# Kernel optimization log

Measured on AMD Instinct MI355X. Metric: run time of the kernel, lower is better.

Reference implementation:

```python
import jax, jax.numpy as jnp
import numpy as np
from jax import lax

R = 3
D = (2 * R + 1) ** 2  # 49 local offsets


def _unfold(x, r):
    # torch F.unfold(kernel=2r+1, padding=r): (B,C,H,W) -> (B, C*K*K, H, W),
    # channel-major (c, ky, kx) ordering, matching conv_general_dilated_patches.
    k = 2 * r + 1
    return lax.conv_general_dilated_patches(
        x, (k, k), (1, 1), [(r, r), (r, r)],
        dimension_numbers=("NCHW", "OIHW", "NCHW"))


def _l2norm(x, eps=1e-12):
    n = jnp.sqrt(jnp.sum(x * x, axis=1, keepdims=True))
    return x / jnp.maximum(n, eps)


def setup_inputs() -> dict:
    key = jax.random.key(0)
    ks = jax.random.split(key, 8)
    B, Cin, Cmid, H, W = 2, 256, 128, 112, 112
    phi_cur = jax.random.normal(ks[0], (B, Cin, H, W), jnp.float32)
    phi_rnd = jax.random.normal(ks[1], (B, Cin, H, W), jnp.float32)
    P_cur = jax.random.normal(ks[2], (B, 3, H, W), jnp.float32)
    P_rnd = jax.random.normal(ks[3], (B, 3, H, W), jnp.float32)
    Wq = jax.random.normal(ks[4], (Cmid, Cin), jnp.float32) * 0.05
    Wk = jax.random.normal(ks[5], (Cmid, Cin), jnp.float32) * 0.05
    Wv = jax.random.normal(ks[6], (D, D), jnp.float32) * 0.1
    bv = jnp.zeros((D,), jnp.float32)
    gamma = jnp.array(1.0, jnp.float32)
    return dict(phi_cur=phi_cur, phi_rnd=phi_rnd, P_cur=P_cur, P_rnd=P_rnd,
                Wq=Wq, Wk=Wk, Wv=Wv, bv=bv, gamma=gamma)


def reference(phi_cur, phi_rnd, P_cur, P_rnd, Wq, Wk, Wv, bv, gamma):
    B, _, H, W = phi_cur.shape
    # 1x1 convs + channel L2 normalize
    q = _l2norm(jnp.einsum('oc,bchw->bohw', Wq, phi_cur))
    k = _l2norm(jnp.einsum('oc,bchw->bohw', Wk, phi_rnd))
    # local cost volume: patches (B, Cmid, D, H, W)
    patches = _unfold(k, R).reshape(B, -1, D, H, W)
    corr = jnp.einsum('bchw,bcdhw->bdhw', q, patches)  # (B,D,H,W)
    vol_corr = jnp.einsum('ed,bdhw->behw', Wv, corr) + bv[None, :, None, None]
    # geometric bias
    Pr = _unfold(P_rnd, R).reshape(B, 3, D, H, W)
    dP = P_cur[:, :, None, :, :] - Pr  # (B,3,D,H,W)
    dz = dP[:, 2]
    dist = jnp.sqrt(jnp.clip(jnp.sum(dP * dP, axis=1), 1e-12, None))
    logits = vol_corr + gamma * (-dist - 0.5 * jnp.abs(dz))
    w = jax.nn.softmax(logits, axis=1)
    off = jnp.arange(-R, R + 1, dtype=w.dtype)
    dY, dX = jnp.meshgrid(off, off, indexing='ij')
    offx = dX.reshape(1, D, 1, 1)
    offy = dY.reshape(1, D, 1, 1)
    du = jnp.sum(w * offx, axis=1, keepdims=True)
    dv = jnp.sum(w * offy, axis=1, keepdims=True)
    conf = jnp.max(w, axis=1, keepdims=True)
    return du, dv, conf
```

## Files before the change

### kernel.cpp

```cpp
#include <hip/hip_runtime.h>
#include <hip/hip_bf16.h>
#include <math.h>

constexpr int B    = 2;
constexpr int CIN  = 256;
constexpr int CMID = 128;
constexpr int H    = 112;
constexpr int W    = 112;
constexpr int HW   = H * W;
constexpr int NPIX = B * HW;
constexpr int RAD  = 3;
constexpr int KS   = 7;
constexpr int DD   = 49;

typedef __attribute__((ext_vector_type(8))) short  short8;
typedef __attribute__((ext_vector_type(4))) float  float4v;

__device__ __forceinline__ unsigned pkbf(float a, float b) {
    __hip_bfloat162 h = __float22bfloat162_rn(make_float2(a, b));
    union { __hip_bfloat162 h2; unsigned u; } c;
    c.h2 = h;
    return c.u;
}

__global__ __launch_bounds__(256) void prep(
    const float* __restrict__ Wq, const float* __restrict__ Wk,
    const float* __restrict__ Wv,
    unsigned short* __restrict__ wqb, unsigned short* __restrict__ wkb,
    float* __restrict__ wvp)
{
    if (blockIdx.x < 64) {
        const int i  = blockIdx.x * 256 + threadIdx.x;
        const int n4 = (CMID * CIN) / 4;
        const float4 v = (i < n4) ? ((const float4*)Wq)[i] : ((const float4*)Wk)[i - n4];
        uint2 r;
        r.x = pkbf(v.x, v.y);
        r.y = pkbf(v.z, v.w);
        if (i < n4) ((uint2*)wqb)[i] = r;
        else        ((uint2*)wkb)[i - n4] = r;
    } else {
        for (int idx = threadIdx.x; idx < DD * 52; idx += 256) {
            const int r = idx / 52, c = idx % 52;
            wvp[idx] = (c < DD) ? Wv[r * DD + c] : 0.f;
        }
    }
}

constexpr int PSTR = 264;

__global__ __launch_bounds__(256, 4) void proj_mfma(
    const float* __restrict__ phi_cur, const float* __restrict__ phi_rnd,
    const unsigned short* __restrict__ wq_bf, const unsigned short* __restrict__ wk_bf,
    unsigned short* __restrict__ q_ws, unsigned short* __restrict__ k_ws)
{
    __shared__ unsigned short pt[64 * PSTR];
    __shared__ float red[4][64];

    const int tid  = threadIdx.x;
    const int lane = tid & 63;
    const int wv   = __builtin_amdgcn_readfirstlane(tid >> 6);
    const int t    = blockIdx.y;

    const float* __restrict__ phi          = t ? phi_rnd : phi_cur;
    const unsigned short* __restrict__ Wbf = t ? wk_bf : wq_bf;
    unsigned short* __restrict__ outp      = t ? k_ws : q_ws;

    const int pgb = blockIdx.x * 64;
    const int b   = pgb / HW;
    const int pim = pgb % HW;
    const float* pbase = phi + (size_t)b * CIN * HW + pim;

    const int m = lane & 15, quad = lane >> 4;

    short8 af[2][8];
#pragma unroll
    for (int ot = 0; ot < 2; ++ot)
#pragma unroll
        for (int kc = 0; kc < 8; ++kc)
            af[ot][kc] = *(const short8*)(Wbf +
                (size_t)(wv * 32 + ot * 16 + m) * CIN + kc * 32 + quad * 8);

#pragma unroll
    for (int half = 0; half < 2; ++half) {
        float4 va[4], vb[4];
#pragma unroll
        for (int p = 0; p < 4; ++p) {
            const int idx = (half * 4 + p) * 256 + tid;
            const int cp  = idx >> 4;
            const int pq  = idx & 15;
            const int c0  = cp * 2;
            va[p] = *(const float4*)(pbase + (size_t)c0 * HW + pq * 4);
            vb[p] = *(const float4*)(pbase + (size_t)(c0 + 1) * HW + pq * 4);
        }
#pragma unroll
        for (int p = 0; p < 4; ++p) {
            const int idx = (half * 4 + p) * 256 + tid;
            const int cp  = idx >> 4;
            const int pq  = idx & 15;
            const int c0  = cp * 2;
            const int swz = ((pq >> 1) & 3) << 3;
            const int col = c0 ^ swz;
            *(unsigned*)(pt + (pq * 4 + 0) * PSTR + col) = pkbf(va[p].x, vb[p].x);
            *(unsigned*)(pt + (pq * 4 + 1) * PSTR + col) = pkbf(va[p].y, vb[p].y);
            *(unsigned*)(pt + (pq * 4 + 2) * PSTR + col) = pkbf(va[p].z, vb[p].z);
            *(unsigned*)(pt + (pq * 4 + 3) * PSTR + col) = pkbf(va[p].w, vb[p].w);
        }
    }

    __syncthreads();

    float4v acc[2][4];
#pragma unroll
    for (int ot = 0; ot < 2; ++ot)
#pragma unroll
        for (int nt = 0; nt < 4; ++nt) acc[ot][nt] = (float4v)0.f;

#pragma unroll
    for (int kc = 0; kc < 8; ++kc) {
        short8 bfr[4];
#pragma unroll
        for (int nt = 0; nt < 4; ++nt) {
            const int row = nt * 16 + m;
            const int col = (kc * 32 + quad * 8) ^ (((row >> 3) & 3) << 3);
            bfr[nt] = *(const short8*)(pt + row * PSTR + col);
        }
#pragma unroll
        for (int nt = 0; nt < 4; ++nt) {
            acc[0][nt] = __builtin_amdgcn_mfma_f32_16x16x32_bf16(af[0][kc], bfr[nt], acc[0][nt], 0, 0, 0);
            acc[1][nt] = __builtin_amdgcn_mfma_f32_16x16x32_bf16(af[1][kc], bfr[nt], acc[1][nt], 0, 0, 0);
        }
    }

#pragma unroll
    for (int nt = 0; nt < 4; ++nt) {
        float ss = 0.f;
#pragma unroll
        for (int ot = 0; ot < 2; ++ot)
#pragma unroll
            for (int r = 0; r < 4; ++r)
                ss = fmaf(acc[ot][nt][r], acc[ot][nt][r], ss);
        ss += __shfl_xor(ss, 16, 64);
        ss += __shfl_xor(ss, 32, 64);
        if (quad == 0) red[wv][nt * 16 + m] = ss;
    }
    __syncthreads();

    float inv[4];
#pragma unroll
    for (int nt = 0; nt < 4; ++nt) {
        const int px = nt * 16 + m;
        const float tot = red[0][px] + red[1][px] + red[2][px] + red[3][px];
        inv[nt] = 1.f / fmaxf(sqrtf(tot), 1e-12f);
    }

#pragma unroll
    for (int nt = 0; nt < 4; ++nt)
#pragma unroll
        for (int ot = 0; ot < 2; ++ot) {
            uint2 st;
            st.x = pkbf(acc[ot][nt][0] * inv[nt], acc[ot][nt][1] * inv[nt]);
            st.y = pkbf(acc[ot][nt][2] * inv[nt], acc[ot][nt][3] * inv[nt]);
            *(uint2*)(outp + (size_t)(pgb + nt * 16 + m) * CMID
                      + wv * 32 + ot * 16 + quad * 4) = st;
        }
}

constexpr int TILE = 16;
constexpr int COLS = TILE + 6;
constexpr int NV   = KS * COLS;
constexpr int KSTR = 136;

__global__ __launch_bounds__(256, 3) void corr_kernel(
    const unsigned short* __restrict__ q_ws, const unsigned short* __restrict__ k_ws,
    const float* __restrict__ P_cur, const float* __restrict__ P_rnd,
    const float* __restrict__ wvp, const float* __restrict__ bv,
    const float* __restrict__ gamma_p, float* __restrict__ out)
{
    __shared__ unsigned short kt[NV * KSTR];
    __shared__ alignas(16) unsigned short qt[TILE * KSTR];
    __shared__ float cs[TILE][52];

    const int tid  = threadIdx.x;
    const int lane = tid & 63;
    const int wv   = __builtin_amdgcn_readfirstlane(tid >> 6);

    const int fid = (blockIdx.z * H + blockIdx.y) * (W / TILE) + blockIdx.x;
    const int swz = (fid & 7) * 196 + (fid >> 3);
    const int b   = swz / (H * (W / TILE));
    const int rem = swz % (H * (W / TILE));
    const int h   = rem / (W / TILE);
    const int w0  = (rem % (W / TILE)) * TILE;

    const int sub  = tid & 15;
    const int vgrp = tid >> 4;
    uint4 stv[10];
#pragma unroll
    for (int pass = 0; pass < 10; ++pass) {
        const int vi = pass * 16 + vgrp;
        uint4 v = make_uint4(0, 0, 0, 0);
        if (vi < NV) {
            const int rr = vi / COLS;
            const int cc = vi % COLS;
            const int hh = h + rr - RAD;
            const int ww = w0 + cc - RAD;
            if (hh >= 0 && hh < H && ww >= 0 && ww < W)
                v = *(const uint4*)(k_ws + (size_t)(b * HW + hh * W + ww) * CMID + sub * 8);
        }
        stv[pass] = v;
    }
    const uint4 qv = *(const uint4*)(q_ws + (size_t)(b * HW + h * W + w0 + vgrp) * CMID + sub * 8);

    const int  ld    = (lane < DD) ? lane : 0;
    const bool valid = (lane < DD);
    float4 wq4[13];
#pragma unroll
    for (int j = 0; j < 13; ++j)
        wq4[j] = *(const float4*)(wvp + ld * 52 + j * 4);
    const float bvv   = bv[ld];
    const float gamma = gamma_p[0];

    const int dy = ld / KS - RAD;
    const int dx = ld % KS - RAD;
    float geo[4];
#pragma unroll
    for (int i = 0; i < 4; ++i) {
        const int pl = wv * 4 + i;
        const int hn = h + dy, wn = w0 + pl + dx;
        const bool inb = valid && hn >= 0 && hn < H && wn >= 0 && wn < W;
        const float* pc = P_cur + (size_t)b * 3 * HW + (h * W + w0 + pl);
        const float cx = pc[0], cy = pc[HW], cz = pc[2 * HW];
        float rx = 0.f, ry = 0.f, rz = 0.f;
        if (inb) {
            const float* pr = P_rnd + (size_t)b * 3 * HW + (hn * W + wn);
            rx = pr[0]; ry = pr[HW]; rz = pr[2 * HW];
        }
        const float dpx = cx - rx, dpy = cy - ry, dpz = cz - rz;
        const float dist = sqrtf(fmaxf(dpx * dpx + dpy * dpy + dpz * dpz, 1e-12f));
        geo[i] = gamma * (-dist - 0.5f * fabsf(dpz));
    }

#pragma unroll
    for (int pass = 0; pass < 10; ++pass) {
        const int vi = pass * 16 + vgrp;
        if (vi < NV)
            *(uint4*)(kt + vi * KSTR + sub * 8) = stv[pass];
    }
    *(uint4*)(qt + vgrp * KSTR + sub * 8) = qv;

    __syncthreads();

    if (tid < TILE * 3)
        cs[tid / 3][49 + tid % 3] = 0.f;

    const int m = lane & 15, quad = lane >> 4;
    for (int g = wv; g < 14; g += 4) {
        const int r  = g >> 1;
        const int nt = g & 1;
        const int vi = min(r * COLS + nt * 16 + m, NV - 1);
        float4v acc = (float4v)0.f;
#pragma unroll
        for (int kc = 0; kc < 4; ++kc) {
            const short8 afrag = *(const short8*)(qt + m * KSTR + kc * 32 + quad * 8);
            const short8 bfrag = *(const short8*)(kt + vi * KSTR + kc * 32 + quad * 8);
            acc = __builtin_amdgcn_mfma_f32_16x16x32_bf16(afrag, bfrag, acc, 0, 0, 0);
        }
#pragma unroll
        for (int reg = 0; reg < 4; ++reg) {
            const int p   = quad * 4 + reg;
            const int off = nt * 16 + m - p;
            if (off >= 0 && off <= 6)
                cs[p][r * 7 + off] = acc[reg];
        }
    }
    __syncthreads();
    float* lsf = reinterpret_cast<float*>(qt);

#pragma unroll
    for (int i = 0; i < 4; ++i) {
        const int pl = wv * 4 + i;
        float logit = -INFINITY;
        if (valid) {
            float va0 = bvv, va1 = 0.f;
#pragma unroll
            for (int e4 = 0; e4 < 13; ++e4) {
                const float4 c4 = *(const float4*)&cs[pl][e4 * 4];
                const float4 w4 = wq4[e4];
                if (e4 & 1) {
                    va1 = fmaf(w4.x, c4.x, va1);
                    va1 = fmaf(w4.y, c4.y, va1);
                    va1 = fmaf(w4.z, c4.z, va1);
                    va1 = fmaf(w4.w, c4.w, va1);
                } else {
                    va0 = fmaf(w4.x, c4.x, va0);
                    va0 = fmaf(w4.y, c4.y, va0);
                    va0 = fmaf(w4.z, c4.z, va0);
                    va0 = fmaf(w4.w, c4.w, va0);
                }
            }
            logit = (va0 + va1) + geo[i];
        }
        lsf[pl * 64 + lane] = logit;
    }

    {
        const int pli = lane >> 4;
        const int dq  = lane & 15;
        const int pl  = wv * 4 + pli;

        const float4 v = ((const float4*)lsf)[pl * 16 + dq];

        float m4 = fmaxf(fmaxf(v.x, v.y), fmaxf(v.z, v.w));
#pragma unroll
        for (int s = 1; s < 16; s <<= 1)
            m4 = fmaxf(m4, __shfl_xor(m4, s, 64));

        const float e0 = __expf(v.x - m4);
        const float e1 = __expf(v.y - m4);
        const float e2 = __expf(v.z - m4);
        const float e3 = __expf(v.w - m4);
        float Z = (e0 + e1) + (e2 + e3);

        const int c0i = dq * 4;
        float dus = 0.f, dvs = 0.f;
        {
            const float ex[4] = { e0, e1, e2, e3 };
#pragma unroll
            for (int j = 0; j < 4; ++j) {
                const int col = c0i + j;
                dus = fmaf(ex[j], (float)(col % KS - RAD), dus);
                dvs = fmaf(ex[j], (float)(col / KS - RAD), dvs);
            }
        }
#pragma unroll
        for (int s = 1; s < 16; s <<= 1) {
            Z   += __shfl_xor(Z,   s, 64);
            dus += __shfl_xor(dus, s, 64);
            dvs += __shfl_xor(dvs, s, 64);
        }

        if (dq == 0) {
            const int pg = b * HW + h * W + w0 + pl;
            const float invZ = 1.f / Z;
            out[pg]            = dus * invZ;
            out[NPIX + pg]     = dvs * invZ;
            out[2 * NPIX + pg] = invZ;
        }
    }
}

extern "C" void kernel_launch(void* const* d_in, const int* in_sizes, int n_in,
                              void* d_out, int out_size, void* d_ws, size_t ws_size,
                              hipStream_t stream)
{
    const float* phi_cur = (const float*)d_in[0];
    const float* phi_rnd = (const float*)d_in[1];
    const float* P_cur   = (const float*)d_in[2];
    const float* P_rnd   = (const float*)d_in[3];
    const float* Wq      = (const float*)d_in[4];
    const float* Wk      = (const float*)d_in[5];
    const float* Wv      = (const float*)d_in[6];
    const float* bv      = (const float*)d_in[7];
    const float* gm      = (const float*)d_in[8];
    float* out = (float*)d_out;

    unsigned short* ws   = (unsigned short*)d_ws;
    unsigned short* q_ws = ws;
    unsigned short* k_ws = q_ws + (size_t)NPIX * CMID;
    unsigned short* wqb  = k_ws + (size_t)NPIX * CMID;
    unsigned short* wkb  = wqb + (size_t)CMID * CIN;
    float*          wvp  = (float*)(wkb + (size_t)CMID * CIN);

    prep<<<dim3(65), 256, 0, stream>>>(Wq, Wk, Wv, wqb, wkb, wvp);

    proj_mfma<<<dim3(NPIX / 64, 2), 256, 0, stream>>>(
        phi_cur, phi_rnd, wqb, wkb, q_ws, k_ws);

    corr_kernel<<<dim3(W / TILE, H, B), 256, 0, stream>>>(
        q_ws, k_ws, P_cur, P_rnd, wvp, bv, gm, out);
}
```

Measured before the change: 132.4 us.

## Fold weight prep into projection kernel and load corr MFMA operands from global

Removes the separate prep launch. The projection kernel now converts the fp32 Wq/Wk rows to bf16 in registers, and one extra block column pads Wv into wvp. The correlation kernel no longer stages k/q tiles in LDS: each wave loads its MFMA fragments straight from global memory, prefetching the next group's B fragments, and splits the accumulation into two chains. This cuts LDS use and one sync and raises occupancy to 4 blocks per SM, at the cost of redundant global reads of overlapping k rows and per-block weight conversion.

```diff
diff --git a/kernel.cpp b/kernel.cpp
--- a/kernel.cpp
+++ b/kernel.cpp
@@ -23,47 +23,36 @@
     return c.u;
 }
 
-__global__ __launch_bounds__(256) void prep(
+constexpr int PSTR = 264;
+
+__global__ __launch_bounds__(256, 4) void proj_mfma(
+    const float* __restrict__ phi_cur, const float* __restrict__ phi_rnd,
     const float* __restrict__ Wq, const float* __restrict__ Wk,
     const float* __restrict__ Wv,
-    unsigned short* __restrict__ wqb, unsigned short* __restrict__ wkb,
+    unsigned short* __restrict__ q_ws, unsigned short* __restrict__ k_ws,
     float* __restrict__ wvp)
 {
-    if (blockIdx.x < 64) {
-        const int i  = blockIdx.x * 256 + threadIdx.x;
-        const int n4 = (CMID * CIN) / 4;
-        const float4 v = (i < n4) ? ((const float4*)Wq)[i] : ((const float4*)Wk)[i - n4];
-        uint2 r;
-        r.x = pkbf(v.x, v.y);
-        r.y = pkbf(v.z, v.w);
-        if (i < n4) ((uint2*)wqb)[i] = r;
-        else        ((uint2*)wkb)[i - n4] = r;
-    } else {
-        for (int idx = threadIdx.x; idx < DD * 52; idx += 256) {
-            const int r = idx / 52, c = idx % 52;
-            wvp[idx] = (c < DD) ? Wv[r * DD + c] : 0.f;
-        }
-    }
-}
-
-constexpr int PSTR = 264;
-
-__global__ __launch_bounds__(256, 4) void proj_mfma(
-    const float* __restrict__ phi_cur, const float* __restrict__ phi_rnd,
-    const unsigned short* __restrict__ wq_bf, const unsigned short* __restrict__ wk_bf,
-    unsigned short* __restrict__ q_ws, unsigned short* __restrict__ k_ws)
-{
+    const int tid  = threadIdx.x;
+    const int t    = blockIdx.y;
+
+    if (blockIdx.x == NPIX / 64) {
+        if (t == 0)
+            for (int idx = tid; idx < DD * 52; idx += 256) {
+                const int r = idx / 52, c = idx % 52;
+                wvp[idx] = (c < DD) ? Wv[r * DD + c] : 0.f;
+            }
+        return;
+    }
+
     __shared__ unsigned short pt[64 * PSTR];
     __shared__ float red[4][64];
 
-    const int tid  = threadIdx.x;
     const int lane = tid & 63;
     const int wv   = __builtin_amdgcn_readfirstlane(tid >> 6);
-    const int t    = blockIdx.y;
-
-    const float* __restrict__ phi          = t ? phi_rnd : phi_cur;
-    const unsigned short* __restrict__ Wbf = t ? wk_bf : wq_bf;
-    unsigned short* __restrict__ outp      = t ? k_ws : q_ws;
+
+    const float* __restrict__ phi = t ? phi_rnd : phi_cur;
+    const float* __restrict__ Wf  = t ? Wk : Wq;
+    unsigned short* __restrict__ outp = t ? k_ws : q_ws;
 
     const int pgb = blockIdx.x * 64;
     const int b   = pgb / HW;
@@ -74,11 +63,24 @@
 
     short8 af[2][8];
 #pragma unroll
-    for (int ot = 0; ot < 2; ++ot)
-#pragma unroll
-        for (int kc = 0; kc < 8; ++kc)
-            af[ot][kc] = *(const short8*)(Wbf +
-                (size_t)(wv * 32 + ot * 16 + m) * CIN + kc * 32 + quad * 8);
+    for (int ot = 0; ot < 2; ++ot) {
+        float4 wt[16];
+        const float* wr = Wf + (size_t)(wv * 32 + ot * 16 + m) * CIN + quad * 8;
+#pragma unroll
+        for (int kc = 0; kc < 8; ++kc) {
+            wt[2 * kc]     = *(const float4*)(wr + kc * 32);
+            wt[2 * kc + 1] = *(const float4*)(wr + kc * 32 + 4);
+        }
+#pragma unroll
+        for (int kc = 0; kc < 8; ++kc) {
+            union { short8 s; unsigned u[4]; } cv;
+            cv.u[0] = pkbf(wt[2 * kc].x,     wt[2 * kc].y);
+            cv.u[1] = pkbf(wt[2 * kc].z,     wt[2 * kc].w);
+            cv.u[2] = pkbf(wt[2 * kc + 1].x, wt[2 * kc + 1].y);
+            cv.u[3] = pkbf(wt[2 * kc + 1].z, wt[2 * kc + 1].w);
+            af[ot][kc] = cv.s;
+        }
+    }
 
 #pragma unroll
     for (int half = 0; half < 2; ++half) {
@@ -167,18 +169,15 @@
 
 constexpr int TILE = 16;
 constexpr int COLS = TILE + 6;
-constexpr int NV   = KS * COLS;
-constexpr int KSTR = 136;
-
-__global__ __launch_bounds__(256, 3) void corr_kernel(
+
+__global__ __launch_bounds__(256, 4) void corr_kernel(
     const unsigned short* __restrict__ q_ws, const unsigned short* __restrict__ k_ws,
     const float* __restrict__ P_cur, const float* __restrict__ P_rnd,
     const float* __restrict__ wvp, const float* __restrict__ bv,
     const float* __restrict__ gamma_p, float* __restrict__ out)
 {
-    __shared__ unsigned short kt[NV * KSTR];
-    __shared__ alignas(16) unsigned short qt[TILE * KSTR];
-    __shared__ float cs[TILE][52];
+    __shared__ alignas(16) float cs[TILE][52];
+    __shared__ alignas(16) float lsf[TILE][64];
 
     const int tid  = threadIdx.x;
     const int lane = tid & 63;
@@ -191,34 +190,40 @@
     const int h   = rem / (W / TILE);
     const int w0  = (rem % (W / TILE)) * TILE;
 
-    const int sub  = tid & 15;
-    const int vgrp = tid >> 4;
-    uint4 stv[10];
-#pragma unroll
-    for (int pass = 0; pass < 10; ++pass) {
-        const int vi = pass * 16 + vgrp;
-        uint4 v = make_uint4(0, 0, 0, 0);
-        if (vi < NV) {
-            const int rr = vi / COLS;
-            const int cc = vi % COLS;
-            const int hh = h + rr - RAD;
-            const int ww = w0 + cc - RAD;
-            if (hh >= 0 && hh < H && ww >= 0 && ww < W)
-                v = *(const uint4*)(k_ws + (size_t)(b * HW + hh * W + ww) * CMID + sub * 8);
-        }
-        stv[pass] = v;
-    }
-    const uint4 qv = *(const uint4*)(q_ws + (size_t)(b * HW + h * W + w0 + vgrp) * CMID + sub * 8);
+    const int m = lane & 15, quad = lane >> 4;
+
+    const size_t qbase = (size_t)b * HW + h * W + w0;
+    short8 aq[4];
+#pragma unroll
+    for (int kc = 0; kc < 4; ++kc)
+        aq[kc] = *(const short8*)(q_ws + (qbase + m) * CMID + kc * 32 + quad * 8);
+
+    auto loadB = [&](int g, short8* dst) {
+        const int r   = g >> 1, nt2 = g & 1;
+        const int cc  = nt2 * 16 + m;
+        const int hh  = h + r - RAD;
+        const int ww  = w0 + cc - RAD;
+        const bool ok = (unsigned)hh < (unsigned)H && (unsigned)ww < (unsigned)W
+                        && cc < COLS;
+        const unsigned short* kp = k_ws
+            + ((size_t)b * HW + (ok ? hh * W + ww : 0)) * CMID + quad * 8;
+#pragma unroll
+        for (int kc = 0; kc < 4; ++kc) {
+            short8 v = *(const short8*)(kp + kc * 32);
+            dst[kc] = ok ? v : (short8)(short)0;
+        }
+    };
+
+    short8 bcur[4], bnxt[4];
+    loadB(wv, bcur);
+
+    if (tid < TILE * 3)
+        cs[tid / 3][49 + tid % 3] = 0.f;
 
     const int  ld    = (lane < DD) ? lane : 0;
     const bool valid = (lane < DD);
-    float4 wq4[13];
-#pragma unroll
-    for (int j = 0; j < 13; ++j)
-        wq4[j] = *(const float4*)(wvp + ld * 52 + j * 4);
+    const float gamma = gamma_p[0];
     const float bvv   = bv[ld];
-    const float gamma = gamma_p[0];
-
     const int dy = ld / KS - RAD;
     const int dx = ld % KS - RAD;
     float geo[4];
@@ -240,40 +245,37 @@
     }
 
 #pragma unroll
-    for (int pass = 0; pass < 10; ++pass) {
-        const int vi = pass * 16 + vgrp;
-        if (vi < NV)
-            *(uint4*)(kt + vi * KSTR + sub * 8) = stv[pass];
-    }
-    *(uint4*)(qt + vgrp * KSTR + sub * 8) = qv;
+    for (int gi = 0; gi < 4; ++gi) {
+        const int g = wv + gi * 4;
+        if (g < 14) {
+            if (g + 4 < 14) loadB(g + 4, bnxt);
+            float4v a0 = (float4v)0.f, a1 = (float4v)0.f;
+            a0 = __builtin_amdgcn_mfma_f32_16x16x32_bf16(aq[0], bcur[0], a0, 0, 0, 0);
+            a1 = __builtin_amdgcn_mfma_f32_16x16x32_bf16(aq[2], bcur[2], a1, 0, 0, 0);
+            a0 = __builtin_amdgcn_mfma_f32_16x16x32_bf16(aq[1], bcur[1], a0, 0, 0, 0);
+            a1 = __builtin_amdgcn_mfma_f32_16x16x32_bf16(aq[3], bcur[3], a1, 0, 0, 0);
+#pragma unroll
+            for (int r4 = 0; r4 < 4; ++r4) a0[r4] += a1[r4];
+            const int r   = g >> 1;
+            const int cc  = (g & 1) * 16 + m;
+#pragma unroll
+            for (int reg = 0; reg < 4; ++reg) {
+                const int p   = quad * 4 + reg;
+                const int off = cc - p;
+                if (off >= 0 && off <= 6)
+                    cs[p][r * 7 + off] = a0[reg];
+            }
+#pragma unroll
+            for (int kc = 0; kc < 4; ++kc) bcur[kc] = bnxt[kc];
+        }
+    }
 
     __syncthreads();
 
-    if (tid < TILE * 3)
-        cs[tid / 3][49 + tid % 3] = 0.f;
-
-    const int m = lane & 15, quad = lane >> 4;
-    for (int g = wv; g < 14; g += 4) {
-        const int r  = g >> 1;
-        const int nt = g & 1;
-        const int vi = min(r * COLS + nt * 16 + m, NV - 1);
-        float4v acc = (float4v)0.f;
-#pragma unroll
-        for (int kc = 0; kc < 4; ++kc) {
-            const short8 afrag = *(const short8*)(qt + m * KSTR + kc * 32 + quad * 8);
-            const short8 bfrag = *(const short8*)(kt + vi * KSTR + kc * 32 + quad * 8);
-            acc = __builtin_amdgcn_mfma_f32_16x16x32_bf16(afrag, bfrag, acc, 0, 0, 0);
-        }
-#pragma unroll
-        for (int reg = 0; reg < 4; ++reg) {
-            const int p   = quad * 4 + reg;
-            const int off = nt * 16 + m - p;
-            if (off >= 0 && off <= 6)
-                cs[p][r * 7 + off] = acc[reg];
-        }
-    }
-    __syncthreads();
-    float* lsf = reinterpret_cast<float*>(qt);
+    float4 wq4[13];
+#pragma unroll
+    for (int j = 0; j < 13; ++j)
+        wq4[j] = *(const float4*)(wvp + ld * 52 + j * 4);
 
 #pragma unroll
     for (int i = 0; i < 4; ++i) {
@@ -299,7 +301,7 @@
             }
             logit = (va0 + va1) + geo[i];
         }
-        lsf[pl * 64 + lane] = logit;
+        lsf[pl][lane] = logit;
     }
 
     {
@@ -307,7 +309,7 @@
         const int dq  = lane & 15;
         const int pl  = wv * 4 + pli;
 
-        const float4 v = ((const float4*)lsf)[pl * 16 + dq];
+        const float4 v = *(const float4*)&lsf[pl][dq * 4];
 
         float m4 = fmaxf(fmaxf(v.x, v.y), fmaxf(v.z, v.w));
 #pragma unroll
@@ -366,14 +368,10 @@
     unsigned short* ws   = (unsigned short*)d_ws;
     unsigned short* q_ws = ws;
     unsigned short* k_ws = q_ws + (size_t)NPIX * CMID;
-    unsigned short* wqb  = k_ws + (size_t)NPIX * CMID;
-    unsigned short* wkb  = wqb + (size_t)CMID * CIN;
-    float*          wvp  = (float*)(wkb + (size_t)CMID * CIN);
-
-    prep<<<dim3(65), 256, 0, stream>>>(Wq, Wk, Wv, wqb, wkb, wvp);
-
-    proj_mfma<<<dim3(NPIX / 64, 2), 256, 0, stream>>>(
-        phi_cur, phi_rnd, wqb, wkb, q_ws, k_ws);
+    float*          wvp  = (float*)(k_ws + (size_t)NPIX * CMID);
+
+    proj_mfma<<<dim3(NPIX / 64 + 1, 2), 256, 0, stream>>>(
+        phi_cur, phi_rnd, Wq, Wk, Wv, q_ws, k_ws, wvp);
 
     corr_kernel<<<dim3(W / TILE, H, B), 256, 0, stream>>>(
         q_ws, k_ws, P_cur, P_rnd, wvp, bv, gm, out);
```

Result: slower. 139.9 us (+5.7%).
